# Optimization experiments

Measured on AMD Instinct MI355X. Metric: run time of the kernel, lower is better.

The kernel has to match this reference:

```python
import jax, jax.numpy as jnp
import numpy as np

B, S, N, H, C = 64, 512, 24, 768, 6

CONST_LAST = jnp.array([0.1, 0.1, 0.1, 0.3, 0.8, 0.01], dtype=jnp.float32)
CONST_MID = jnp.array([0.1, 0.1, 0.1, 0.8, 0.3, 0.01], dtype=jnp.float32)


def setup_inputs() -> dict:
    key = jax.random.key(0)
    k1, k2, k3, k4 = jax.random.split(key, 4)
    last_hidden_state = jax.random.normal(k1, (B, S, H), dtype=jnp.float32)
    # strictly increasing boundaries in [0, S-1]: sort randint in [0, S-N) then add arange(N)
    base = jnp.sort(jax.random.randint(k2, (B, N), 0, S - N), axis=1)
    sentence_token = base + jnp.arange(N, dtype=base.dtype)[None, :]
    W = jax.random.normal(k3, (C, H), dtype=jnp.float32) * 0.02
    b = jax.random.normal(k4, (C,), dtype=jnp.float32) * 0.02
    return {"last_hidden_state": last_hidden_state, "sentence_token": sentence_token,
            "W": W, "b": b}


def reference(last_hidden_state, sentence_token, W, b):
    # last_hidden_state: [B,S,H]; sentence_token: [B,N] strictly increasing boundaries.
    # Segment j covers tokens [prev+1, t_j] inclusive (prev = -1 for j==0).
    ends = sentence_token                                            # [B,N]
    prev = jnp.concatenate([-jnp.ones_like(ends[:, :1]), ends[:, :-1]], axis=1)
    # prefix sums with leading zero: csp[:, t+1] = sum of tokens 0..t
    cs = jnp.cumsum(last_hidden_state, axis=1)                       # [B,S,H]
    csp = jnp.concatenate([jnp.zeros_like(cs[:, :1]), cs], axis=1)   # [B,S+1,H]
    seg_sum = (jnp.take_along_axis(csp, (ends + 1)[:, :, None], axis=1)
               - jnp.take_along_axis(csp, (prev + 1)[:, :, None], axis=1))  # [B,N,H]
    lens = (ends - prev).astype(last_hidden_state.dtype)[:, :, None]  # >= 1 by construction
    seg_mean = seg_sum / lens                                         # [B,N,H]
    probs = jax.nn.sigmoid(jnp.einsum('bnh,ch->bnc', seg_mean, W) + b)  # [B,N,C]
    # override: boundary > 500 -> constant probability vector (different if last sentence)
    is_last = (jnp.arange(ends.shape[1]) == ends.shape[1] - 1)[None, :, None]  # [1,N,1]
    const = jnp.where(is_last, CONST_LAST[None, None, :], CONST_MID[None, None, :])
    over = (ends > 500)[:, :, None]
    return jnp.where(over, const, probs)
```

## Files before the change

### kernel.cpp

```cpp
#include <hip/hip_runtime.h>
#include <math.h>

#define B_ 64
#define S_ 512
#define N_ 24
#define H_ 768
#define C_ 6

template <int CTRL>
__device__ __forceinline__ float dpp_add(float v) {
  int x = __builtin_amdgcn_update_dpp(0, __float_as_int(v), CTRL, 0xF, 0xF, true);
  return v + __int_as_float(x);
}
__device__ __forceinline__ float wave_sum(float v) {
  v = dpp_add<0xB1>(v);
  v = dpp_add<0x4E>(v);
  v = dpp_add<0x141>(v);
  v = dpp_add<0x140>(v);
  v += __shfl_xor(v, 16, 64);
  v += __shfl_xor(v, 32, 64);
  return v;
}

__global__ __launch_bounds__(256, 4) void proj_kernel(
    const float* __restrict__ lhs, const float* __restrict__ W,
    float* __restrict__ Y) {
  const int tid = threadIdx.x;
  const int lane = tid & 63;
  const int gwave = (int)((blockIdx.x * 256 + tid) >> 6);
  const int t_base = gwave * 4;

  const float4* W4 = (const float4*)W;
  float4 w[3][C_];
#pragma unroll
  for (int k = 0; k < 3; ++k)
#pragma unroll
    for (int c = 0; c < C_; ++c)
      w[k][c] = W4[c * (H_ / 4) + k * 64 + lane];
#pragma unroll
  for (int k = 0; k < 3; ++k)
    asm volatile("" : "+v"(w[k][0].x), "+v"(w[k][0].y), "+v"(w[k][0].z), "+v"(w[k][0].w),
                       "+v"(w[k][1].x), "+v"(w[k][1].y), "+v"(w[k][1].z), "+v"(w[k][1].w),
                       "+v"(w[k][2].x), "+v"(w[k][2].y), "+v"(w[k][2].z), "+v"(w[k][2].w),
                       "+v"(w[k][3].x), "+v"(w[k][3].y), "+v"(w[k][3].z), "+v"(w[k][3].w),
                       "+v"(w[k][4].x), "+v"(w[k][4].y), "+v"(w[k][4].z), "+v"(w[k][4].w),
                       "+v"(w[k][5].x), "+v"(w[k][5].y), "+v"(w[k][5].z), "+v"(w[k][5].w));

  const float4* x4 = (const float4*)(lhs + (size_t)t_base * H_);

#pragma unroll
  for (int r = 0; r < 2; ++r) {
    float4 x0[3], x1[3];
#pragma unroll
    for (int k = 0; k < 3; ++k) x0[k] = x4[r * 384 + k * 64 + lane];
#pragma unroll
    for (int k = 0; k < 3; ++k) x1[k] = x4[r * 384 + 192 + k * 64 + lane];

#pragma unroll
    for (int tt = 0; tt < 2; ++tt) {
      const float4* xx = tt ? x1 : x0;
      float y[C_];
#pragma unroll
      for (int c = 0; c < C_; ++c) y[c] = 0.f;
#pragma unroll
      for (int k = 0; k < 3; ++k)
#pragma unroll
        for (int c = 0; c < C_; ++c)
          y[c] += xx[k].x * w[k][c].x + xx[k].y * w[k][c].y +
                  xx[k].z * w[k][c].z + xx[k].w * w[k][c].w;
#pragma unroll
      for (int c = 0; c < C_; ++c) y[c] = wave_sum(y[c]);
      float out = y[0];
      out = (lane == 1) ? y[1] : out;
      out = (lane == 2) ? y[2] : out;
      out = (lane == 3) ? y[3] : out;
      out = (lane == 4) ? y[4] : out;
      out = (lane == 5) ? y[5] : out;
      const int t = t_base + r * 2 + tt;
      if (lane < C_) Y[(size_t)t * C_ + lane] = out;
    }
  }
}

__global__ __launch_bounds__(256) void seg_finalize(
    const float* __restrict__ Y, const int* __restrict__ st,
    const float* __restrict__ bias, float* __restrict__ out) {
  __shared__ float ly[S_ * C_];
  __shared__ int lst[N_];
  __shared__ float lb[C_];
  const int tid = threadIdx.x;
  const int b = blockIdx.x;

  const float4* Y4 = (const float4*)(Y + (size_t)b * S_ * C_);
  float4* ly4 = (float4*)ly;
#pragma unroll
  for (int i = 0; i < 3; ++i) ly4[i * 256 + tid] = Y4[i * 256 + tid];
  if (tid < N_) lst[tid] = st[b * N_ + tid];
  if (tid < C_) lb[tid] = bias[tid];
  __syncthreads();

  if (tid < N_ * C_) {
    const int j = tid / C_;
    const int c = tid % C_;
    const int end = lst[j];
    const int prev = (j == 0) ? -1 : lst[j - 1];
    float s = 0.f;
    for (int k = prev + 1; k <= end; ++k) s += ly[k * C_ + c];
    float logit = s / (float)(end - prev) + lb[c];
    float p = 1.0f / (1.0f + expf(-logit));
    if (end > 500) {
      float cl = (c < 3) ? 0.1f : (c == 3 ? 0.3f : (c == 4 ? 0.8f : 0.01f));
      float cm = (c < 3) ? 0.1f : (c == 3 ? 0.8f : (c == 4 ? 0.3f : 0.01f));
      p = (j == N_ - 1) ? cl : cm;
    }
    out[b * N_ * C_ + tid] = p;
  }
}

extern "C" void kernel_launch(void* const* d_in, const int* in_sizes, int n_in,
                              void* d_out, int out_size, void* d_ws, size_t ws_size,
                              hipStream_t stream) {
  const float* lhs  = (const float*)d_in[0];
  const int*   st   = (const int*)d_in[1];
  const float* W    = (const float*)d_in[2];
  const float* bias = (const float*)d_in[3];
  float* Y = (float*)d_ws;

  proj_kernel<<<2048, 256, 0, stream>>>(lhs, W, Y);
  seg_finalize<<<B_, 256, 0, stream>>>(Y, st, bias, (float*)d_out);
}
```

Measured before the change: 157.4 us.

## Segment-sum tokens before projecting and skip tokens past the last boundary

Reorders the computation so tokens are first summed per segment, using chunked blocks that accumulate with atomics into a zeroed workspace, and the 768-wide projection then runs only once per segment instead of once per token. Tokens after the last sentence boundary are never read, which cuts HBM traffic on the bandwidth-bound input. The cost is a memset, float atomics whose summation order is nondeterministic, and a third launch.

```diff
diff --git a/kernel.cpp b/kernel.cpp
--- a/kernel.cpp
+++ b/kernel.cpp
@@ -6,6 +6,51 @@
 #define N_ 24
 #define H_ 768
 #define C_ 6
+#define CHUNKS2 32
+#define TOK (S_ / CHUNKS2)
+
+__global__ __launch_bounds__(192) void seg_sum_kernel(
+    const float* __restrict__ lhs, const int* __restrict__ st,
+    float* __restrict__ segsum) {
+  __shared__ int lst[N_];
+  const int tid = threadIdx.x;
+  const int b = blockIdx.x / CHUNKS2;
+  const int chunk = blockIdx.x % CHUNKS2;
+  if (tid < N_) lst[tid] = st[b * N_ + tid];
+  __syncthreads();
+  const int last = lst[N_ - 1];
+  const int s0 = chunk * TOK;
+  if (s0 > last) return;
+  const int s_stop = min(s0 + TOK, last + 1);
+
+  int j = 0;
+  while (lst[j] < s0) ++j;
+
+  const float4* X4 = (const float4*)lhs + ((size_t)b * S_ + s0) * (H_ / 4) + tid;
+  float4 acc = make_float4(0.f, 0.f, 0.f, 0.f);
+  bool dirty = false;
+  float4 x = X4[0];
+  for (int s = s0; s < s_stop; ++s) {
+    float4 xn = make_float4(0.f, 0.f, 0.f, 0.f);
+    if (s + 1 < s_stop) xn = X4[(size_t)(s - s0 + 1) * (H_ / 4)];
+    acc.x += x.x; acc.y += x.y; acc.z += x.z; acc.w += x.w;
+    dirty = true;
+    if (s == lst[j]) {
+      float* dst = segsum + ((size_t)(b * N_ + j) * (H_ / 4) + tid) * 4;
+      atomicAdd(dst + 0, acc.x); atomicAdd(dst + 1, acc.y);
+      atomicAdd(dst + 2, acc.z); atomicAdd(dst + 3, acc.w);
+      acc = make_float4(0.f, 0.f, 0.f, 0.f);
+      dirty = false;
+      ++j;
+    }
+    x = xn;
+  }
+  if (dirty) {
+    float* dst = segsum + ((size_t)(b * N_ + j) * (H_ / 4) + tid) * 4;
+    atomicAdd(dst + 0, acc.x); atomicAdd(dst + 1, acc.y);
+    atomicAdd(dst + 2, acc.z); atomicAdd(dst + 3, acc.w);
+  }
+}
 
 template <int CTRL>
 __device__ __forceinline__ float dpp_add(float v) {
@@ -22,98 +67,49 @@
   return v;
 }
 
-__global__ __launch_bounds__(256, 4) void proj_kernel(
-    const float* __restrict__ lhs, const float* __restrict__ W,
-    float* __restrict__ Y) {
-  const int tid = threadIdx.x;
-  const int lane = tid & 63;
-  const int gwave = (int)((blockIdx.x * 256 + tid) >> 6);
-  const int t_base = gwave * 4;
+__global__ __launch_bounds__(64) void proj_out_kernel(
+    const float* __restrict__ segsum, const int* __restrict__ st,
+    const float* __restrict__ W, const float* __restrict__ bias,
+    float* __restrict__ out) {
+  const int lane = threadIdx.x;
+  const int bj = blockIdx.x;
+  const int b = bj / N_;
+  const int j = bj % N_;
+  const int end = st[b * N_ + j];
+  const int prev = (j == 0) ? -1 : st[b * N_ + j - 1];
 
+  const float4* X4 = (const float4*)segsum + (size_t)bj * (H_ / 4);
   const float4* W4 = (const float4*)W;
-  float4 w[3][C_];
+  float4 x0 = X4[lane], x1 = X4[64 + lane], x2 = X4[128 + lane];
+  float y[C_];
 #pragma unroll
-  for (int k = 0; k < 3; ++k)
+  for (int c = 0; c < C_; ++c) {
+    float4 w0 = W4[c * (H_ / 4) + lane];
+    float4 w1 = W4[c * (H_ / 4) + 64 + lane];
+    float4 w2 = W4[c * (H_ / 4) + 128 + lane];
+    y[c] = x0.x * w0.x + x0.y * w0.y + x0.z * w0.z + x0.w * w0.w +
+           x1.x * w1.x + x1.y * w1.y + x1.z * w1.z + x1.w * w1.w +
+           x2.x * w2.x + x2.y * w2.y + x2.z * w2.z + x2.w * w2.w;
+  }
 #pragma unroll
-    for (int c = 0; c < C_; ++c)
-      w[k][c] = W4[c * (H_ / 4) + k * 64 + lane];
-#pragma unroll
-  for (int k = 0; k < 3; ++k)
-    asm volatile("" : "+v"(w[k][0].x), "+v"(w[k][0].y), "+v"(w[k][0].z), "+v"(w[k][0].w),
-                       "+v"(w[k][1].x), "+v"(w[k][1].y), "+v"(w[k][1].z), "+v"(w[k][1].w),
-                       "+v"(w[k][2].x), "+v"(w[k][2].y), "+v"(w[k][2].z), "+v"(w[k][2].w),
-                       "+v"(w[k][3].x), "+v"(w[k][3].y), "+v"(w[k][3].z), "+v"(w[k][3].w),
-                       "+v"(w[k][4].x), "+v"(w[k][4].y), "+v"(w[k][4].z), "+v"(w[k][4].w),
-                       "+v"(w[k][5].x), "+v"(w[k][5].y), "+v"(w[k][5].z), "+v"(w[k][5].w));
+  for (int c = 0; c < C_; ++c) y[c] = wave_sum(y[c]);
 
-  const float4* x4 = (const float4*)(lhs + (size_t)t_base * H_);
-
-#pragma unroll
-  for (int r = 0; r < 2; ++r) {
-    float4 x0[3], x1[3];
-#pragma unroll
-    for (int k = 0; k < 3; ++k) x0[k] = x4[r * 384 + k * 64 + lane];
-#pragma unroll
-    for (int k = 0; k < 3; ++k) x1[k] = x4[r * 384 + 192 + k * 64 + lane];
-
-#pragma unroll
-    for (int tt = 0; tt < 2; ++tt) {
-      const float4* xx = tt ? x1 : x0;
-      float y[C_];
-#pragma unroll
-      for (int c = 0; c < C_; ++c) y[c] = 0.f;
-#pragma unroll
-      for (int k = 0; k < 3; ++k)
-#pragma unroll
-        for (int c = 0; c < C_; ++c)
-          y[c] += xx[k].x * w[k][c].x + xx[k].y * w[k][c].y +
-                  xx[k].z * w[k][c].z + xx[k].w * w[k][c].w;
-#pragma unroll
-      for (int c = 0; c < C_; ++c) y[c] = wave_sum(y[c]);
-      float out = y[0];
-      out = (lane == 1) ? y[1] : out;
-      out = (lane == 2) ? y[2] : out;
-      out = (lane == 3) ? y[3] : out;
-      out = (lane == 4) ? y[4] : out;
-      out = (lane == 5) ? y[5] : out;
-      const int t = t_base + r * 2 + tt;
-      if (lane < C_) Y[(size_t)t * C_ + lane] = out;
-    }
-  }
-}
-
-__global__ __launch_bounds__(256) void seg_finalize(
-    const float* __restrict__ Y, const int* __restrict__ st,
-    const float* __restrict__ bias, float* __restrict__ out) {
-  __shared__ float ly[S_ * C_];
-  __shared__ int lst[N_];
-  __shared__ float lb[C_];
-  const int tid = threadIdx.x;
-  const int b = blockIdx.x;
-
-  const float4* Y4 = (const float4*)(Y + (size_t)b * S_ * C_);
-  float4* ly4 = (float4*)ly;
-#pragma unroll
-  for (int i = 0; i < 3; ++i) ly4[i * 256 + tid] = Y4[i * 256 + tid];
-  if (tid < N_) lst[tid] = st[b * N_ + tid];
-  if (tid < C_) lb[tid] = bias[tid];
-  __syncthreads();
-
-  if (tid < N_ * C_) {
-    const int j = tid / C_;
-    const int c = tid % C_;
-    const int end = lst[j];
-    const int prev = (j == 0) ? -1 : lst[j - 1];
-    float s = 0.f;
-    for (int k = prev + 1; k <= end; ++k) s += ly[k * C_ + c];
-    float logit = s / (float)(end - prev) + lb[c];
+  if (lane < C_) {
+    const int c = lane;
+    float v = y[0];
+    v = (c == 1) ? y[1] : v;
+    v = (c == 2) ? y[2] : v;
+    v = (c == 3) ? y[3] : v;
+    v = (c == 4) ? y[4] : v;
+    v = (c == 5) ? y[5] : v;
+    float logit = v / (float)(end - prev) + bias[c];
     float p = 1.0f / (1.0f + expf(-logit));
     if (end > 500) {
       float cl = (c < 3) ? 0.1f : (c == 3 ? 0.3f : (c == 4 ? 0.8f : 0.01f));
       float cm = (c < 3) ? 0.1f : (c == 3 ? 0.8f : (c == 4 ? 0.3f : 0.01f));
       p = (j == N_ - 1) ? cl : cm;
     }
-    out[b * N_ * C_ + tid] = p;
+    out[bj * C_ + c] = p;
   }
 }
 
@@ -124,8 +120,9 @@
   const int*   st   = (const int*)d_in[1];
   const float* W    = (const float*)d_in[2];
   const float* bias = (const float*)d_in[3];
-  float* Y = (float*)d_ws;
+  float* segsum = (float*)d_ws;
 
-  proj_kernel<<<2048, 256, 0, stream>>>(lhs, W, Y);
-  seg_finalize<<<B_, 256, 0, stream>>>(Y, st, bias, (float*)d_out);
+  hipMemsetAsync(d_ws, 0, (size_t)B_ * N_ * H_ * sizeof(float), stream);
+  seg_sum_kernel<<<B_ * CHUNKS2, 192, 0, stream>>>(lhs, st, segsum);
+  proj_out_kernel<<<B_ * N_, 64, 0, stream>>>(segsum, st, W, bias, (float*)d_out);
 }
```

Result: slower. 172.9 us (+9.8%).
